# Kernel tuning notes

Hardware: AMD Instinct MI355X
Metric: run time of the kernel (lower is better)

Reference implementation:

```python
import jax, jax.numpy as jnp
import numpy as np

NEG = -9.0e15
D = 768


def _init_params(key, d):
    ks = jax.random.split(key, 12)
    s = 0.02
    p = {}
    p['Wa'] = jax.random.normal(ks[0], (d, 1), jnp.float32) * s
    p['ba'] = jnp.zeros((1,), jnp.float32)
    for i, name in enumerate(['qs', 'ks', 'qc', 'kc', 'qr', 'kr']):
        p['W' + name] = jax.random.normal(ks[1 + i], (d, d), jnp.float32) * s
        p['b' + name] = jnp.zeros((d,), jnp.float32)
    p['Wf1'] = jax.random.normal(ks[8], (3 * d, d), jnp.float32) * s
    p['bf1'] = jnp.zeros((d,), jnp.float32)
    p['Wf2'] = jax.random.normal(ks[9], (d, d), jnp.float32) * s
    p['bf2'] = jnp.zeros((d,), jnp.float32)
    p['gamma'] = jnp.ones((d,), jnp.float32)
    p['beta'] = jnp.zeros((d,), jnp.float32)
    return p


def setup_inputs() -> dict:
    key = jax.random.key(0)
    k1, k2, k3 = jax.random.split(key, 3)
    B, L = 8, 1024
    inp = {
        'x': jax.random.normal(k1, (B, L, D), jnp.float32),
        'x_ids': jax.random.randint(k2, (B, L), 0, 1000, jnp.int64 if jax.config.read('jax_enable_x64') else jnp.int32).astype(jnp.int32),
        'pad_idx': 0,
    }
    inp.update(_init_params(k3, D))
    return inp


def _forward(x, x_ids, pad_idx, Wa, ba, Wqs, bqs, Wks, bks, Wqc, bqc, Wkc, bkc,
             Wqr, bqr, Wkr, bkr, Wf1, bf1, Wf2, bf2, gamma, beta):
    B, L, d = x.shape
    valid = x_ids != pad_idx                             # [B,L]
    valid_len = valid.sum(axis=1)
    sep_pos = jnp.clip(valid_len // 2, 1, max(1, L - 2))  # [B]
    pos = jnp.arange(L)[None, :]                          # [1,L]
    false_mask = (pos < sep_pos[:, None]) & valid         # [B,L]
    option_mask = (pos > sep_pos[:, None]) & valid        # [B,L]

    # anomaly gate over false segment
    a_logits = (x @ Wa + ba)[..., 0]                      # [B,L]
    a_logits = jnp.where(false_mask, a_logits, NEG)
    gate = jax.nn.softmax(a_logits, axis=1) * false_mask.astype(x.dtype)
    gate = gate / jnp.clip(gate.sum(axis=1, keepdims=True), 1e-8)

    scale = 1.0 / jnp.sqrt(jnp.asarray(d, x.dtype))
    q_sup, k_sup = x @ Wqs + bqs, x @ Wks + bks
    q_con, k_con = x @ Wqc + bqc, x @ Wkc + bkc
    q_rep, k_rep = x @ Wqr + bqr, x @ Wkr + bkr

    sup_s = jnp.einsum('bld,bmd->blm', q_sup, k_sup) * scale
    con_s = jnp.einsum('bld,bmd->blm', q_con, k_con) * scale
    rep_s = jnp.einsum('bld,bmd->blm', q_rep, k_rep) * scale

    pair_mask = false_mask[:, :, None] & option_mask[:, None, :]  # [B,L,L]
    sup_attn = jax.nn.softmax(jnp.where(pair_mask, sup_s, NEG), axis=-1)
    rep_attn = jax.nn.softmax(jnp.where(pair_mask, rep_s + jnp.tanh(con_s), NEG), axis=-1)

    rep_vec = jnp.einsum('blm,bmd->bld', rep_attn, x)
    sup_vec = jnp.einsum('blm,bmd->bld', sup_attn, x)

    anomaly_false = jnp.einsum('bl,bld->bd', gate, x)
    w_rep = jnp.einsum('bl,bld->bd', gate, rep_vec)
    w_sup = jnp.einsum('bl,bld->bd', gate, sup_vec)

    fused = jnp.concatenate([anomaly_false, w_rep, w_sup], axis=-1)
    fused = jnp.maximum(fused @ Wf1 + bf1, 0.0) @ Wf2 + bf2  # dropout = eval identity

    mu = fused.mean(axis=-1, keepdims=True)
    var = ((fused - mu) ** 2).mean(axis=-1, keepdims=True)
    fused = (fused - mu) / jnp.sqrt(var + 1e-5) * gamma + beta
    return fused


def reference(x, x_ids, pad_idx, Wa, ba, Wqs, bqs, Wks, bks, Wqc, bqc, Wkc, bkc,
              Wqr, bqr, Wkr, bkr, Wf1, bf1, Wf2, bf2, gamma, beta):
    return _forward(x, x_ids, pad_idx, Wa, ba, Wqs, bqs, Wks, bks, Wqc, bqc,
                    Wkc, bkc, Wqr, bqr, Wkr, bkr, Wf1, bf1, Wf2, bf2, gamma, beta)
```

## Files before the change

### kernel.cpp

```cpp
#include <hip/hip_runtime.h>
#include <math.h>

#define L 1024
#define NB 8
#define D 768
#define NEGV (-9.0e15f)
#define SCALE 0.036084391824351615f

typedef unsigned short u16;
typedef __attribute__((ext_vector_type(8))) short short8;
typedef __attribute__((ext_vector_type(4))) float float4v;
#define MFMA_BF16 __builtin_amdgcn_mfma_f32_16x16x32_bf16

__device__ __forceinline__ float b2f(u16 u) {
    union { unsigned int i; float f; } v; v.i = ((unsigned int)u) << 16; return v.f;
}
__device__ __forceinline__ u16 f2b(float f) {
    union { float fv; unsigned int i; } v; v.fv = f;
    unsigned int x = v.i;
    x += 0x7fffu + ((x >> 16) & 1u);
    return (u16)(x >> 16);
}

template<int F32>
__device__ __forceinline__ float4 ld4(const void* p, size_t idx) {
    if (F32) return *(const float4*)((const float*)p + idx);
    ushort4 v = *(const ushort4*)((const u16*)p + idx);
    return make_float4(b2f(v.x), b2f(v.y), b2f(v.z), b2f(v.w));
}
template<int F32>
__device__ __forceinline__ float ld1(const void* p, size_t idx) {
    if (F32) return ((const float*)p)[idx];
    return b2f(((const u16*)p)[idx]);
}
__device__ __forceinline__ int ldid(const int* p, size_t idx, int is64) {
    return is64 ? p[idx * 2] : p[idx];
}

#define WS_FLAG  ((size_t)0)
#define WS_SEP   ((size_t)64)
#define WS_C0    ((size_t)128)
#define WS_Z0    ((size_t)192)
#define WS_W1    ((size_t)9472)
#define WS_GATE  ((size_t)18752)
#define WS_CSUP  ((size_t)51520)
#define WS_CREP  ((size_t)84288)
#define WS_AF    ((size_t)117056)
#define WS_WREP  ((size_t)141632)
#define WS_WSUP  ((size_t)166208)
#define WS_HACC  ((size_t)190784)
#define WS_ALOG  ((size_t)215360)
#define WS_T     ((size_t)248128)
#define WS_OACC  ((size_t)303104)
#define WS_XB    ((size_t)524288)
#define WS_Z     ((size_t)13107200)
#define WS_SSUP  ((size_t)31981568)
#define WS_WB    WS_SSUP
#define WS_SCMB  ((size_t)40370176)
#define WS_M     WS_SCMB

struct PP { const void* W[6]; const void* b[6]; };

__global__ __launch_bounds__(128) void kdetect(const void* x, const void* ids, int* flag) {
    __shared__ int cnt[2];
    int tid = threadIdx.x;
    if (tid == 0) { cnt[0] = 0; cnt[1] = 0; }
    __syncthreads();
    if (tid < 64) {
        u16 u = ((const u16*)x)[tid * 2];
        int e = (u >> 7) & 0xFF;
        if (e >= 100 && e <= 140) atomicAdd(&cnt[0], 1);
    } else {
        int v = ((const int*)ids)[(tid - 64) * 2 + 1];
        if (v != 0) atomicAdd(&cnt[1], 1);
    }
    __syncthreads();
    if (tid == 0) {
        flag[0] = (cnt[0] < 32) ? 1 : 0;
        flag[1] = (cnt[1] == 0) ? 1 : 0;
    }
}

template<int F32> __device__ void kbias_body(const void* W, const void* vec,
        float* out, float* vs) {
    int tid = threadIdx.x;
    for (int i = tid; i < D; i += 256) vs[i] = ld1<F32>(vec, i);
    __syncthreads();
    int row = blockIdx.x * 64 + (tid >> 2);
    int sub = tid & 3;
    float acc = 0.f;
    for (int i = 0; i < 48; ++i) {
        int k = i * 16 + sub * 4;
        float4 wv = ld4<F32>(W, (size_t)row * D + k);
        acc += wv.x * vs[k] + wv.y * vs[k + 1] + wv.z * vs[k + 2] + wv.w * vs[k + 3];
    }
    acc += __shfl_xor(acc, 1);
    acc += __shfl_xor(acc, 2);
    if (sub == 0) out[row] = acc;
}
template<int F32> __device__ void kc0_body(const void* bq, const void* bk,
        float* c0, float* red) {
    int tid = threadIdx.x;
    float s = 0.f;
    for (int i = tid; i < D; i += 256) s += ld1<F32>(bq, i) * ld1<F32>(bk, i);
    red[tid] = s; __syncthreads();
    for (int st = 128; st > 0; st >>= 1) { if (tid < st) red[tid] += red[tid + st]; __syncthreads(); }
    if (tid == 0) c0[0] = red[0];
}
__global__ __launch_bounds__(256) void kbias_row(PP pp, float* z0, float* w1,
        float* c0, const int* flag) {
    __shared__ float vs[D];
    __shared__ float red[256];
    int y = blockIdx.y;
    if (y == 4) {
        if (blockIdx.x != 0) return;
        if (flag[0]) kc0_body<1>(pp.b[2], pp.b[3], c0, red);
        else         kc0_body<0>(pp.b[2], pp.b[3], c0, red);
        return;
    }
    const void* W; const void* vec; float* out;
    if (y < 3) { W = pp.W[2 * y + 1]; vec = pp.b[2 * y]; out = z0 + y * D; }
    else       { W = pp.W[2];         vec = pp.b[3];     out = w1; }
    if (flag[0]) kbias_body<1>(W, vec, out, vs);
    else         kbias_body<0>(W, vec, out, vs);
}

template<int F32> __device__ void kx_body(const void* x, const void* Wa,
        const void* ba, const float* w1, const float* c0, u16* xb, float* alog,
        float* tbuf, float* ws2) {
    int tid = threadIdx.x;
    for (int i = tid; i < D; i += 256) {
        ws2[i]     = ld1<F32>(Wa, i);
        ws2[D + i] = w1[i];
    }
    __syncthreads();
    int row = blockIdx.x * 32 + (tid >> 3);
    int sub = tid & 7;
    float a0 = 0.f, a1 = 0.f;
    for (int i = 0; i < 24; ++i) {
        int k = i * 32 + sub * 4;
        float4 xv = ld4<F32>(x, (size_t)row * D + k);
        ushort4 o;
        o.x = f2b(xv.x); o.y = f2b(xv.y); o.z = f2b(xv.z); o.w = f2b(xv.w);
        *(ushort4*)(xb + (size_t)row * D + k) = o;
        a0 += xv.x * ws2[k] + xv.y * ws2[k + 1] + xv.z * ws2[k + 2] + xv.w * ws2[k + 3];
        a1 += xv.x * ws2[D + k] + xv.y * ws2[D + k + 1] + xv.z * ws2[D + k + 2] + xv.w * ws2[D + k + 3];
    }
    #pragma unroll
    for (int d = 1; d < 8; d <<= 1) {
        a0 += __shfl_xor(a0, d); a1 += __shfl_xor(a1, d);
    }
    int b = row >> 10, l = row & 1023;
    if (sub == 0) alog[row] = a0 + ld1<F32>(ba, 0);
    else if (sub == 1 && l < 512) tbuf[(size_t)b * 512 + l] = a1 + c0[0];
}
__global__ __launch_bounds__(256) void kx(const void* x, PP pp, const void* Wa,
        const void* ba, const float* w1, const float* c0, u16* xb, u16* Wb,
        float* alog, float* tbuf, const int* flag) {
    __shared__ float ws2[2 * D];
    int bid = blockIdx.x;
    if (bid < 256) {
        if (flag[0]) kx_body<1>(x, Wa, ba, w1, c0, xb, alog, tbuf, ws2);
        else         kx_body<0>(x, Wa, ba, w1, c0, xb, alog, tbuf, ws2);
        return;
    }
    int t = (bid - 256) / 288, inner = (bid - 256) % 288;
    const void* src = pp.W[t];
    u16* dst = Wb + (size_t)t * D * D;
    size_t base = ((size_t)inner * 256 + threadIdx.x) * 8;
    if (flag[0]) {
        float4 a = *(const float4*)((const float*)src + base);
        float4 b = *(const float4*)((const float*)src + base + 4);
        uint4 o; u16* po = (u16*)&o;
        po[0] = f2b(a.x); po[1] = f2b(a.y); po[2] = f2b(a.z); po[3] = f2b(a.w);
        po[4] = f2b(b.x); po[5] = f2b(b.y); po[6] = f2b(b.z); po[7] = f2b(b.w);
        *(uint4*)(dst + base) = o;
    } else {
        *(uint4*)(dst + base) = *(const uint4*)((const u16*)src + base);
    }
}

__global__ __launch_bounds__(256) void k0b(const int* __restrict__ ids,
        const int* __restrict__ padp, const float* __restrict__ alog,
        float* __restrict__ gate, int* __restrict__ sepArr,
        float* __restrict__ af, float* __restrict__ wrep, float* __restrict__ wsup,
        float* __restrict__ hacc, float* __restrict__ oacc,
        float* __restrict__ csup, float* __restrict__ crep,
        const int* __restrict__ flag) {
    __shared__ float red[256];
    __shared__ int sepSh;
    int is64 = flag[1];
    int b = blockIdx.x, tid = threadIdx.x;
    int pad = padp[0];
    int cnt = 0;
    for (int l = tid; l < L; l += 256) cnt += (ldid(ids, (size_t)b * L + l, is64) != pad) ? 1 : 0;
    red[tid] = (float)cnt; __syncthreads();
    for (int s = 128; s > 0; s >>= 1) { if (tid < s) red[tid] += red[tid + s]; __syncthreads(); }
    if (tid == 0) {
        int vl = (int)red[0];
        int sep = vl / 2; if (sep < 1) sep = 1; if (sep > L - 2) sep = L - 2;
        sepSh = sep; sepArr[b] = sep;
    }
    __syncthreads();
    int sep = sepSh;
    float lv[4]; int lidx[4];
    float mx = -3.4e38f;
    for (int u = 0; u < 4; ++u) {
        int l = tid + u * 256; lidx[u] = l;
        bool fm = (l < sep) && (ldid(ids, (size_t)b * L + l, is64) != pad);
        float v = fm ? alog[b * L + l] : NEGV;
        lv[u] = v; mx = fmaxf(mx, v);
    }
    red[tid] = mx; __syncthreads();
    for (int s = 128; s > 0; s >>= 1) { if (tid < s) red[tid] = fmaxf(red[tid], red[tid + s]); __syncthreads(); }
    mx = red[0]; __syncthreads();
    float se = 0.f;
    for (int u = 0; u < 4; ++u) { lv[u] = expf(lv[u] - mx); se += lv[u]; }
    red[tid] = se; __syncthreads();
    for (int s = 128; s > 0; s >>= 1) { if (tid < s) red[tid] += red[tid + s]; __syncthreads(); }
    float den = fmaxf(red[0], 1e-30f); __syncthreads();
    float gs = 0.f; float gv[4];
    for (int u = 0; u < 4; ++u) {
        int l = lidx[u];
        bool fm = (l < sep) && (ldid(ids, (size_t)b * L + l, is64) != pad);
        float p = lv[u] / den;
        gv[u] = fm ? p : 0.f;
        gs += gv[u];
    }
    red[tid] = gs; __syncthreads();
    for (int s = 128; s > 0; s >>= 1) { if (tid < s) red[tid] += red[tid + s]; __syncthreads(); }
    gs = red[0];
    float inv = 1.f / fmaxf(gs, 1e-8f);
    for (int u = 0; u < 4; ++u) gate[b * L + lidx[u]] = gv[u] * inv;
    for (int l = tid; l < L; l += 256) { csup[b * L + l] = 0.f; crep[b * L + l] = 0.f; }
    for (int i = tid; i < D; i += 256) {
        af[b * D + i] = 0.f; wrep[b * D + i] = 0.f; wsup[b * D + i] = 0.f;
        hacc[b * D + i] = 0.f; oacc[b * D + i] = 0.f;
    }
}

__device__ __forceinline__ void stage128_async(const u16* __restrict__ G, size_t ld,
        int r0, int k0, u16* S, int tid) {
    int rowa = tid >> 2, koa = (tid & 3) << 3;
    int wave = tid >> 6;
    const u16* g1 = &G[(size_t)(r0 + rowa) * ld + k0 + koa];
    const u16* g2 = &G[(size_t)(r0 + rowa + 64) * ld + k0 + koa];
    __builtin_amdgcn_global_load_lds((__attribute__((address_space(1))) void*)(u16*)g1,
        (__attribute__((address_space(3))) void*)(S + wave * 512), 16, 0, 0);
    __builtin_amdgcn_global_load_lds((__attribute__((address_space(1))) void*)(u16*)g2,
        (__attribute__((address_space(3))) void*)(S + 2048 + wave * 512), 16, 0, 0);
}
__device__ __forceinline__ void stage64_async(const u16* __restrict__ G, size_t ld,
        int r0, int k0, u16* S, int tid) {
    int rowa = tid >> 2, koa = (tid & 3) << 3;
    int wave = tid >> 6;
    const u16* g = &G[(size_t)(r0 + rowa) * ld + k0 + koa];
    __builtin_amdgcn_global_load_lds((__attribute__((address_space(1))) void*)(u16*)g,
        (__attribute__((address_space(3))) void*)(S + wave * 512), 16, 0, 0);
}

__device__ __forceinline__ void gemm_core128(const u16* __restrict__ A, size_t lda, int r0,
        const u16* __restrict__ B, size_t ldb, int c0, int K,
        u16* As, u16* Bs, float4v acc[4][4]) {
    int tid = threadIdx.x;
    int lane = tid & 63, wave = tid >> 6;
    int wm = (wave >> 1) << 6, wn = (wave & 1) << 6;
    int quad = lane >> 4, lrow = lane & 15;
    #pragma unroll
    for (int i = 0; i < 4; ++i)
        #pragma unroll
        for (int j = 0; j < 4; ++j) acc[i][j] = (float4v){0.f, 0.f, 0.f, 0.f};
    for (int k0 = 0; k0 < K; k0 += 64) {
        __syncthreads();
        stage128_async(A, lda, r0, k0, As, tid);
        stage128_async(A, lda, r0, k0 + 32, As + 4096, tid);
        stage128_async(B, ldb, c0, k0, Bs, tid);
        stage128_async(B, ldb, c0, k0 + 32, Bs + 4096, tid);
        __syncthreads();
        #pragma unroll
        for (int p = 0; p < 2; ++p) {
            const u16* Ap = As + p * 4096;
            const u16* Bp = Bs + p * 4096;
            short8 af[4], bf[4];
            #pragma unroll
            for (int i = 0; i < 4; ++i) af[i] = *(const short8*)&Ap[(wm + i * 16 + lrow) * 32 + quad * 8];
            #pragma unroll
            for (int j = 0; j < 4; ++j) bf[j] = *(const short8*)&Bp[(wn + j * 16 + lrow) * 32 + quad * 8];
            #pragma unroll
            for (int i = 0; i < 4; ++i)
                #pragma unroll
                for (int j = 0; j < 4; ++j)
                    acc[i][j] = MFMA_BF16(af[i], bf[j], acc[i][j], 0, 0, 0);
        }
    }
}

__device__ __forceinline__ void gemm_core64(const u16* __restrict__ A, size_t lda, int r0,
        const u16* __restrict__ B, size_t ldb, int c0, int K,
        u16* As, u16* Bs, float4v acc[2][4]) {
    int tid = threadIdx.x;
    int lane = tid & 63, wave = tid >> 6;
    int wm = (wave >> 1) << 5, wn = (wave & 1) << 6;
    int quad = lane >> 4, lrow = lane & 15;
    #pragma unroll
    for (int i = 0; i < 2; ++i)
        #pragma unroll
        for (int j = 0; j < 4; ++j) acc[i][j] = (float4v){0.f, 0.f, 0.f, 0.f};
    for (int k0 = 0; k0 < K; k0 += 64) {
        __syncthreads();
        stage64_async(A, lda, r0, k0, As, tid);
        stage64_async(A, lda, r0, k0 + 32, As + 2048, tid);
        stage128_async(B, ldb, c0, k0, Bs, tid);
        stage128_async(B, ldb, c0, k0 + 32, Bs + 4096, tid);
        __syncthreads();
        #pragma unroll
        for (int p = 0; p < 2; ++p) {
            const u16* Ap = As + p * 2048;
            const u16* Bp = Bs + p * 4096;
            short8 fa[2], fb[4];
            #pragma unroll
            for (int i = 0; i < 2; ++i) fa[i] = *(const short8*)&Ap[(wm + i * 16 + lrow) * 32 + quad * 8];
            #pragma unroll
            for (int j = 0; j < 4; ++j) fb[j] = *(const short8*)&Bp[(wn + j * 16 + lrow) * 32 + quad * 8];
            #pragma unroll
            for (int i = 0; i < 2; ++i)
                #pragma unroll
                for (int j = 0; j < 4; ++j)
                    acc[i][j] = MFMA_BF16(fa[i], fb[j], acc[i][j], 0, 0, 0);
        }
    }
}

__global__ __launch_bounds__(256) void kM_mfma(const u16* __restrict__ Wb, u16* __restrict__ Mt) {
    __shared__ __align__(16) u16 As[128 * 64];
    __shared__ __align__(16) u16 Bs[128 * 64];
    int p = blockIdx.z;
    int r0 = blockIdx.y * 128, c0 = blockIdx.x * 128;
    float4v acc[4][4];
    gemm_core128(Wb + (size_t)(2 * p + 1) * D * D, D, r0,
                 Wb + (size_t)(2 * p) * D * D, D, c0, D, As, Bs, acc);
    int lane = threadIdx.x & 63, wave = threadIdx.x >> 6;
    int wm = (wave >> 1) << 6, wn = (wave & 1) << 6;
    int quad = lane >> 4, lrow = lane & 15;
    u16* out = Mt + (size_t)p * D * D;
    #pragma unroll
    for (int i = 0; i < 4; ++i)
        #pragma unroll
        for (int j = 0; j < 4; ++j) {
            int brow = r0 + wm + i * 16 + quad * 4;
            int col = c0 + wn + j * 16 + lrow;
            #pragma unroll
            for (int r = 0; r < 4; ++r)
                out[(size_t)(brow + r) * D + col] = f2b(acc[i][j][r]);
        }
}

__global__ __launch_bounds__(256) void kZ_mfma(const u16* __restrict__ xb,
        const u16* __restrict__ Mt, const float* __restrict__ z0,
        u16* __restrict__ Zbuf, const int* __restrict__ sepArr) {
    __shared__ __align__(16) u16 As[64 * 64];
    __shared__ __align__(16) u16 Bs[128 * 64];
    int z = blockIdx.z;
    int p = z >> 3, b = z & 7;
    int sep = sepArr[b];
    int r0 = blockIdx.y * 64;
    if (r0 >= sep) return;
    int c0 = blockIdx.x * 128;
    float4v acc[2][4];
    gemm_core64(xb + (size_t)b * L * D, D, r0,
                Mt + (size_t)p * D * D, D, c0, D, As, Bs, acc);
    int lane = threadIdx.x & 63, wave = threadIdx.x >> 6;
    int wm = (wave >> 1) << 5, wn = (wave & 1) << 6;
    int quad = lane >> 4, lrow = lane & 15;
    const float* z0p = z0 + p * D;
    u16* out = Zbuf + ((size_t)p * NB + b) * 512 * D;
    #pragma unroll
    for (int i = 0; i < 2; ++i)
        #pragma unroll
        for (int j = 0; j < 4; ++j) {
            int brow = r0 + wm + i * 16 + quad * 4;
            int col = c0 + wn + j * 16 + lrow;
            float zb = z0p[col];
            #pragma unroll
            for (int r = 0; r < 4; ++r)
                out[(size_t)(brow + r) * D + col] = f2b(acc[i][j][r] + zb);
        }
}

__global__ __launch_bounds__(256) void kS_mfma(const u16* __restrict__ Zbuf,
        const u16* __restrict__ xb, const float* __restrict__ tcbuf,
        const int* __restrict__ sepArr, u16* __restrict__ ssup,
        u16* __restrict__ scmb) {
    __shared__ __align__(16) u16 smem[16384];
    int b = blockIdx.z;
    int sep = sepArr[b];
    int xi = blockIdx.x;
    int tid = threadIdx.x, lane = tid & 63, wave = tid >> 6;
    int quad = lane >> 4, lrow = lane & 15;
    int wm = (wave >> 1) << 5, wn = (wave & 1) << 6;
    int m0 = blockIdx.y * 128;
    if (m0 + 127 <= sep) return;
    u16* A0 = smem;
    u16* A1 = smem + 4096;
    u16* Bs = smem + 8192;
    const u16* X = xb + (size_t)b * L * D;
    if (xi < 8) {
        int l0 = xi * 64;
        if (l0 >= sep) return;
        float4v acc[2][4];
        gemm_core64(Zbuf + (size_t)b * 512 * D, D, l0, X, D, m0, D, A0, Bs, acc);
        u16* out = ssup + (size_t)b * 512 * L;
        #pragma unroll
        for (int i = 0; i < 2; ++i)
            #pragma unroll
            for (int j = 0; j < 4; ++j) {
                int brow = l0 + wm + i * 16 + quad * 4;
                int col = m0 + wn + j * 16 + lrow;
                #pragma unroll
                for (int r = 0; r < 4; ++r)
                    out[(size_t)(brow + r) * L + col] = f2b(acc[i][j][r] * SCALE);
            }
        return;
    }
    int l0 = (xi - 8) * 64;
    if (l0 >= sep) return;
    const u16* Zr = Zbuf + ((size_t)2 * NB + b) * 512 * D;
    const u16* Zc = Zbuf + ((size_t)1 * NB + b) * 512 * D;
    float4v ar_[2][4], ac_[2][4];
    #pragma unroll
    for (int i = 0; i < 2; ++i)
        #pragma unroll
        for (int j = 0; j < 4; ++j) { ar_[i][j] = (float4v){0.f,0.f,0.f,0.f}; ac_[i][j] = (float4v){0.f,0.f,0.f,0.f}; }
    for (int k0 = 0; k0 < D; k0 += 64) {
        __syncthreads();
        stage64_async(Zr, D, l0, k0, A0, tid);
        stage64_async(Zr, D, l0, k0 + 32, A0 + 2048, tid);
        stage64_async(Zc, D, l0, k0, A1, tid);
        stage64_async(Zc, D, l0, k0 + 32, A1 + 2048, tid);
        stage128_async(X, D, m0, k0, Bs, tid);
        stage128_async(X, D, m0, k0 + 32, Bs + 4096, tid);
        __syncthreads();
        #pragma unroll
        for (int p = 0; p < 2; ++p) {
            const u16* Arp = A0 + p * 2048;
            const u16* Acp = A1 + p * 2048;
            const u16* Bp  = Bs + p * 4096;
            short8 fr[2], fc[2], fb[4];
            #pragma unroll
            for (int i = 0; i < 2; ++i) {
                fr[i] = *(const short8*)&Arp[(wm + i * 16 + lrow) * 32 + quad * 8];
                fc[i] = *(const short8*)&Acp[(wm + i * 16 + lrow) * 32 + quad * 8];
            }
            #pragma unroll
            for (int j = 0; j < 4; ++j) fb[j] = *(const short8*)&Bp[(wn + j * 16 + lrow) * 32 + quad * 8];
            #pragma unroll
            for (int i = 0; i < 2; ++i)
                #pragma unroll
                for (int j = 0; j < 4; ++j) {
                    ar_[i][j] = MFMA_BF16(fr[i], fb[j], ar_[i][j], 0, 0, 0);
                    ac_[i][j] = MFMA_BF16(fc[i], fb[j], ac_[i][j], 0, 0, 0);
                }
        }
    }
    const float* tc = tcbuf + (size_t)b * 512;
    u16* out = scmb + (size_t)b * 512 * L;
    #pragma unroll
    for (int i = 0; i < 2; ++i)
        #pragma unroll
        for (int j = 0; j < 4; ++j) {
            int brow = l0 + wm + i * 16 + quad * 4;
            int col = m0 + wn + j * 16 + lrow;
            #pragma unroll
            for (int r = 0; r < 4; ++r) {
                float vv = ar_[i][j][r] * SCALE
                         + tanhf((ac_[i][j][r] + tc[brow + r]) * SCALE);
                out[(size_t)(brow + r) * L + col] = f2b(vv);
            }
        }
}

__global__ __launch_bounds__(256) void k2bc(const u16* __restrict__ ssup,
        const u16* __restrict__ scmb, const int* __restrict__ ids,
        const int* __restrict__ padp, const int* __restrict__ sepArr,
        const float* __restrict__ gate, float* __restrict__ csup,
        float* __restrict__ crep, const int* __restrict__ flag) {
    __shared__ float colacc[4][2][1024];
    int b = blockIdx.y;
    int sep = sepArr[b];
    int l0 = blockIdx.x * 8;
    int tid = threadIdx.x, lane = tid & 63, w = tid >> 6;
    for (int i = tid; i < 4 * 2 * 1024; i += 256) ((float*)colacc)[i] = 0.f;
    __syncthreads();
    if (l0 < sep) {
        int is64 = flag[1];
        int pad = padp[0];
        unsigned int okmask = 0;
        #pragma unroll
        for (int u = 0; u < 16; ++u) {
            int m = u * 64 + lane;
            bool ok = (m > sep) && (ldid(ids, (size_t)b * L + m, is64) != pad);
            okmask |= (ok ? 1u : 0u) << u;
        }
        for (int t = 0; t < 2; ++t) {
            int l = l0 + w * 2 + t;
            if (l >= sep) continue;
            float g = gate[b * L + l];
            if (g == 0.f) continue;
            const u16* rs = ssup + ((size_t)b * 512 + l) * L;
            const u16* rc = scmb + ((size_t)b * 512 + l) * L;
            float s0[16], s1[16];
            float mx0 = -3.4e38f, mx1 = -3.4e38f;
            #pragma unroll
            for (int u = 0; u < 16; ++u) {
                int m = u * 64 + lane;
                bool ok = (okmask >> u) & 1u;
                s0[u] = ok ? b2f(rs[m]) : NEGV;
                s1[u] = ok ? b2f(rc[m]) : NEGV;
                mx0 = fmaxf(mx0, s0[u]); mx1 = fmaxf(mx1, s1[u]);
            }
            #pragma unroll
            for (int d = 1; d < 64; d <<= 1) {
                mx0 = fmaxf(mx0, __shfl_xor(mx0, d));
                mx1 = fmaxf(mx1, __shfl_xor(mx1, d));
            }
            float e0 = 0.f, e1 = 0.f;
            #pragma unroll
            for (int u = 0; u < 16; ++u) {
                s0[u] = expf(s0[u] - mx0); e0 += s0[u];
                s1[u] = expf(s1[u] - mx1); e1 += s1[u];
            }
            #pragma unroll
            for (int d = 1; d < 64; d <<= 1) {
                e0 += __shfl_xor(e0, d);
                e1 += __shfl_xor(e1, d);
            }
            float i0 = g / fmaxf(e0, 1e-30f), i1 = g / fmaxf(e1, 1e-30f);
            #pragma unroll
            for (int u = 0; u < 16; ++u) {
                int m = u * 64 + lane;
                colacc[w][0][m] += s0[u] * i0;
                colacc[w][1][m] += s1[u] * i1;
            }
        }
    }
    __syncthreads();
    for (int m = tid; m < 1024; m += 256) {
        float a0 = colacc[0][0][m] + colacc[1][0][m] + colacc[2][0][m] + colacc[3][0][m];
        float a1 = colacc[0][1][m] + colacc[1][1][m] + colacc[2][1][m] + colacc[3][1][m];
        if (a0 != 0.f) atomicAdd(&csup[b * L + m], a0);
        if (a1 != 0.f) atomicAdd(&crep[b * L + m], a1);
    }
}

__global__ __launch_bounds__(256) void k3(const u16* __restrict__ xb,
        const float* __restrict__ gate, const float* __restrict__ csup,
        const float* __restrict__ crep, float* __restrict__ af,
        float* __restrict__ wrep, float* __restrict__ wsup) {
    int b = blockIdx.y, c = blockIdx.x;
    int tid = threadIdx.x;
    float a0 = 0.f, a1 = 0.f, a2 = 0.f;
    float r0 = 0.f, r1 = 0.f, r2 = 0.f;
    float q0 = 0.f, q1 = 0.f, q2 = 0.f;
    for (int mm = 0; mm < 16; ++mm) {
        int m = c * 16 + mm;
        float wg = gate[b * L + m], wr = crep[b * L + m], wq = csup[b * L + m];
        if (wg == 0.f && wr == 0.f && wq == 0.f) continue;
        size_t base = ((size_t)b * L + m) * D;
        float x0 = b2f(xb[base + tid]);
        float x1 = b2f(xb[base + tid + 256]);
        float x2 = b2f(xb[base + tid + 512]);
        a0 += wg * x0; a1 += wg * x1; a2 += wg * x2;
        r0 += wr * x0; r1 += wr * x1; r2 += wr * x2;
        q0 += wq * x0; q1 += wq * x1; q2 += wq * x2;
    }
    atomicAdd(&af[b * D + tid], a0); atomicAdd(&af[b * D + tid + 256], a1); atomicAdd(&af[b * D + tid + 512], a2);
    atomicAdd(&wrep[b * D + tid], r0); atomicAdd(&wrep[b * D + tid + 256], r1); atomicAdd(&wrep[b * D + tid + 512], r2);
    atomicAdd(&wsup[b * D + tid], q0); atomicAdd(&wsup[b * D + tid + 256], q1); atomicAdd(&wsup[b * D + tid + 512], q2);
}

template<int F32> __device__ void kh1_body(const float* af, const float* wrep,
        const float* wsup, const void* Wf1, float* hacc, float* fs) {
    int tid = threadIdx.x;
    int c0 = blockIdx.x * 128, k0 = blockIdx.y * 144;
    for (int e = tid; e < 8 * 144; e += 256) {
        int b = e / 144, kk = e - b * 144;
        int k = k0 + kk;
        float v = (k < D) ? af[b * D + k] : (k < 2 * D) ? wrep[b * D + k - D]
                                                        : wsup[b * D + k - 2 * D];
        fs[b * 144 + kk] = v;
    }
    __syncthreads();
    int col = c0 + (tid & 127);
    int kg = tid >> 7;
    float acc[NB];
    #pragma unroll
    for (int b = 0; b < NB; ++b) acc[b] = 0.f;
    #pragma unroll 4
    for (int r = 0; r < 72; ++r) {
        int kk = kg * 72 + r;
        float w = ld1<F32>(Wf1, (size_t)(k0 + kk) * D + col);
        #pragma unroll
        for (int b = 0; b < NB; ++b) acc[b] += fs[b * 144 + kk] * w;
    }
    #pragma unroll
    for (int b = 0; b < NB; ++b) atomicAdd(&hacc[b * D + col], acc[b]);
}
__global__ __launch_bounds__(256) void kh1(const float* af, const float* wrep,
        const float* wsup, const void* Wf1, float* hacc, const int* flag) {
    __shared__ float fs[8 * 144];
    if (flag[0]) kh1_body<1>(af, wrep, wsup, Wf1, hacc, fs);
    else         kh1_body<0>(af, wrep, wsup, Wf1, hacc, fs);
}

template<int F32> __device__ void kh2_body(const float* hacc, const void* bf1,
        const void* Wf2, float* oacc, float* hsl) {
    int tid = threadIdx.x;
    int c0 = blockIdx.x * 128, k0 = blockIdx.y * 96;
    for (int e = tid; e < 8 * 96; e += 256) {
        int b = e / 96, kk = e - b * 96;
        int k = k0 + kk;
        hsl[b * 96 + kk] = fmaxf(hacc[b * D + k] + ld1<F32>(bf1, k), 0.f);
    }
    __syncthreads();
    int col = c0 + (tid & 127);
    int kg = tid >> 7;
    float acc[NB];
    #pragma unroll
    for (int b = 0; b < NB; ++b) acc[b] = 0.f;
    #pragma unroll 4
    for (int r = 0; r < 48; ++r) {
        int kk = kg * 48 + r;
        float w = ld1<F32>(Wf2, (size_t)(k0 + kk) * D + col);
        #pragma unroll
        for (int b = 0; b < NB; ++b) acc[b] += hsl[b * 96 + kk] * w;
    }
    #pragma unroll
    for (int b = 0; b < NB; ++b) atomicAdd(&oacc[b * D + col], acc[b]);
}
__global__ __launch_bounds__(256) void kh2(const float* hacc, const void* bf1,
        const void* Wf2, float* oacc, const int* flag) {
    __shared__ float hsl[8 * 96];
    if (flag[0]) kh2_body<1>(hacc, bf1, Wf2, oacc, hsl);
    else         kh2_body<0>(hacc, bf1, Wf2, oacc, hsl);
}

template<int F32> __device__ void kln_body(const float* oacc, const void* bf2,
        const void* gamma, const void* beta, void* out, float* red) {
    int b = blockIdx.x, tid = threadIdx.x;
    float o[3];
    #pragma unroll
    for (int u = 0; u < 3; ++u) {
        int i = tid + u * 256;
        o[u] = oacc[b * D + i] + ld1<F32>(bf2, i);
    }
    red[tid] = o[0] + o[1] + o[2]; __syncthreads();
    for (int s = 128; s > 0; s >>= 1) { if (tid < s) red[tid] += red[tid + s]; __syncthreads(); }
    float mu = red[0] / (float)D; __syncthreads();
    float vs = 0.f;
    #pragma unroll
    for (int u = 0; u < 3; ++u) vs += (o[u] - mu) * (o[u] - mu);
    red[tid] = vs; __syncthreads();
    for (int s = 128; s > 0; s >>= 1) { if (tid < s) red[tid] += red[tid + s]; __syncthreads(); }
    float var = red[0] / (float)D;
    float rstd = 1.0f / sqrtf(var + 1e-5f);
    #pragma unroll
    for (int u = 0; u < 3; ++u) {
        int i = tid + u * 256;
        float v = (o[u] - mu) * rstd * ld1<F32>(gamma, i) + ld1<F32>(beta, i);
        if (F32) ((float*)out)[b * D + i] = v;
        else     ((u16*)out)[b * D + i] = f2b(v);
    }
}
__global__ __launch_bounds__(256) void kln(const float* oacc, const void* bf2,
        const void* gamma, const void* beta, void* out, const int* flag) {
    __shared__ float red[256];
    if (flag[0]) kln_body<1>(oacc, bf2, gamma, beta, out, red);
    else         kln_body<0>(oacc, bf2, gamma, beta, out, red);
}

extern "C" void kernel_launch(void* const* d_in, const int* in_sizes, int n_in,
                              void* d_out, int out_size, void* d_ws, size_t ws_size,
                              hipStream_t stream) {
    const void* x    = d_in[0];
    const int* ids   = (const int*)d_in[1];
    const int* padp  = (const int*)d_in[2];
    const void* Wa   = d_in[3];
    const void* ba   = d_in[4];
    PP pp;
    pp.W[0] = d_in[5];  pp.b[0] = d_in[6];
    pp.W[1] = d_in[7];  pp.b[1] = d_in[8];
    pp.W[2] = d_in[9];  pp.b[2] = d_in[10];
    pp.W[3] = d_in[11]; pp.b[3] = d_in[12];
    pp.W[4] = d_in[13]; pp.b[4] = d_in[14];
    pp.W[5] = d_in[15]; pp.b[5] = d_in[16];
    const void* Wf1 = d_in[17]; const void* bf1 = d_in[18];
    const void* Wf2 = d_in[19]; const void* bf2 = d_in[20];
    const void* gamma = d_in[21]; const void* beta = d_in[22];

    char* ws = (char*)d_ws;
    int*   flag   = (int*)(ws + WS_FLAG);
    int*   sepArr = (int*)(ws + WS_SEP);
    float* c0   = (float*)(ws + WS_C0);
    float* z0   = (float*)(ws + WS_Z0);
    float* w1   = (float*)(ws + WS_W1);
    float* gate = (float*)(ws + WS_GATE);
    float* csup = (float*)(ws + WS_CSUP);
    float* crep = (float*)(ws + WS_CREP);
    float* af   = (float*)(ws + WS_AF);
    float* wrep = (float*)(ws + WS_WREP);
    float* wsup = (float*)(ws + WS_WSUP);
    float* hacc = (float*)(ws + WS_HACC);
    float* oacc = (float*)(ws + WS_OACC);
    float* alog = (float*)(ws + WS_ALOG);
    float* tbuf = (float*)(ws + WS_T);
    u16* xb   = (u16*)(ws + WS_XB);
    u16* Zbuf = (u16*)(ws + WS_Z);
    u16* Wb   = (u16*)(ws + WS_WB);
    u16* Mt   = (u16*)(ws + WS_M);
    u16* ssup = (u16*)(ws + WS_SSUP);
    u16* scmb = (u16*)(ws + WS_SCMB);

    kdetect<<<dim3(1), dim3(128), 0, stream>>>(x, ids, flag);
    kbias_row<<<dim3(12, 5), dim3(256), 0, stream>>>(pp, z0, w1, c0, flag);
    kx<<<dim3(1984), dim3(256), 0, stream>>>(x, pp, Wa, ba, w1, c0, xb, Wb, alog, tbuf, flag);
    k0b<<<dim3(NB), dim3(256), 0, stream>>>(ids, padp, alog, gate, sepArr,
                                            af, wrep, wsup, hacc, oacc, csup, crep, flag);
    kM_mfma<<<dim3(6, 6, 3), dim3(256), 0, stream>>>(Wb, Mt);
    kZ_mfma<<<dim3(6, 8, 24), dim3(256), 0, stream>>>(xb, Mt, z0, Zbuf, sepArr);
    kS_mfma<<<dim3(16, 8, NB), dim3(256), 0, stream>>>(Zbuf, xb, tbuf, sepArr, ssup, scmb);
    k2bc<<<dim3(64, NB), dim3(256), 0, stream>>>(ssup, scmb, ids, padp, sepArr,
                                                 gate, csup, crep, flag);
    k3<<<dim3(64, NB), dim3(256), 0, stream>>>(xb, gate, csup, crep, af, wrep, wsup);
    kh1<<<dim3(6, 16), dim3(256), 0, stream>>>(af, wrep, wsup, Wf1, hacc, flag);
    kh2<<<dim3(6, 8), dim3(256), 0, stream>>>(hacc, bf1, Wf2, oacc, flag);
    kln<<<dim3(NB), dim3(256), 0, stream>>>(oacc, bf2, gamma, beta, d_out, flag);
}
```

Baseline: 286.0 us.

## Fuse weight bf16 conversion into M-matrix GEMM staging, drop Wb buffer

Removes the separate pass in kx that converted the six projection weight matrices to bf16 into a workspace buffer. kM_mfma now reads the fp32 (or bf16) weights directly and converts while staging tiles into shared memory, using its own simpler single-buffered K=32 loop instead of gemm_core128. This saves a full write and re-read of the weight copies and shrinks kx to its x-processing blocks. In exchange the M GEMM reads wider fp32 data, converts each tile redundantly across blocks, and loses whatever pipelining gemm_core128 had.

```diff
diff --git a/kernel.cpp b/kernel.cpp
--- a/kernel.cpp
+++ b/kernel.cpp
@@ -55,7 +55,6 @@
 #define WS_XB    ((size_t)524288)
 #define WS_Z     ((size_t)13107200)
 #define WS_SSUP  ((size_t)31981568)
-#define WS_WB    WS_SSUP
 #define WS_SCMB  ((size_t)40370176)
 #define WS_M     WS_SCMB
 
@@ -154,30 +153,12 @@
     if (sub == 0) alog[row] = a0 + ld1<F32>(ba, 0);
     else if (sub == 1 && l < 512) tbuf[(size_t)b * 512 + l] = a1 + c0[0];
 }
-__global__ __launch_bounds__(256) void kx(const void* x, PP pp, const void* Wa,
-        const void* ba, const float* w1, const float* c0, u16* xb, u16* Wb,
+__global__ __launch_bounds__(256) void kx(const void* x, const void* Wa,
+        const void* ba, const float* w1, const float* c0, u16* xb,
         float* alog, float* tbuf, const int* flag) {
     __shared__ float ws2[2 * D];
-    int bid = blockIdx.x;
-    if (bid < 256) {
-        if (flag[0]) kx_body<1>(x, Wa, ba, w1, c0, xb, alog, tbuf, ws2);
-        else         kx_body<0>(x, Wa, ba, w1, c0, xb, alog, tbuf, ws2);
-        return;
-    }
-    int t = (bid - 256) / 288, inner = (bid - 256) % 288;
-    const void* src = pp.W[t];
-    u16* dst = Wb + (size_t)t * D * D;
-    size_t base = ((size_t)inner * 256 + threadIdx.x) * 8;
-    if (flag[0]) {
-        float4 a = *(const float4*)((const float*)src + base);
-        float4 b = *(const float4*)((const float*)src + base + 4);
-        uint4 o; u16* po = (u16*)&o;
-        po[0] = f2b(a.x); po[1] = f2b(a.y); po[2] = f2b(a.z); po[3] = f2b(a.w);
-        po[4] = f2b(b.x); po[5] = f2b(b.y); po[6] = f2b(b.z); po[7] = f2b(b.w);
-        *(uint4*)(dst + base) = o;
-    } else {
-        *(uint4*)(dst + base) = *(const uint4*)((const u16*)src + base);
-    }
+    if (flag[0]) kx_body<1>(x, Wa, ba, w1, c0, xb, alog, tbuf, ws2);
+    else         kx_body<0>(x, Wa, ba, w1, c0, xb, alog, tbuf, ws2);
 }
 
 __global__ __launch_bounds__(256) void k0b(const int* __restrict__ ids,
@@ -331,18 +312,52 @@
     }
 }
 
-__global__ __launch_bounds__(256) void kM_mfma(const u16* __restrict__ Wb, u16* __restrict__ Mt) {
-    __shared__ __align__(16) u16 As[128 * 64];
-    __shared__ __align__(16) u16 Bs[128 * 64];
-    int p = blockIdx.z;
+template<int F32> __device__ __forceinline__ void stageW(const void* G, size_t ld,
+        int r0, int k0, u16* S, int tid) {
+    int row = tid >> 2, ko = (tid & 3) << 3;
+    #pragma unroll
+    for (int h = 0; h < 2; ++h) {
+        size_t idx = (size_t)(r0 + row + h * 64) * ld + k0 + ko;
+        uint4 o;
+        if (F32) {
+            float4 a = *(const float4*)((const float*)G + idx);
+            float4 b = *(const float4*)((const float*)G + idx + 4);
+            u16* po = (u16*)&o;
+            po[0] = f2b(a.x); po[1] = f2b(a.y); po[2] = f2b(a.z); po[3] = f2b(a.w);
+            po[4] = f2b(b.x); po[5] = f2b(b.y); po[6] = f2b(b.z); po[7] = f2b(b.w);
+        } else {
+            o = *(const uint4*)((const u16*)G + idx);
+        }
+        *(uint4*)&S[(size_t)(row + h * 64) * 32 + ko] = o;
+    }
+}
+template<int F32> __device__ void kM_body(const void* Wk, const void* Wq,
+        u16* out, u16* As, u16* Bs) {
     int r0 = blockIdx.y * 128, c0 = blockIdx.x * 128;
-    float4v acc[4][4];
-    gemm_core128(Wb + (size_t)(2 * p + 1) * D * D, D, r0,
-                 Wb + (size_t)(2 * p) * D * D, D, c0, D, As, Bs, acc);
-    int lane = threadIdx.x & 63, wave = threadIdx.x >> 6;
+    int tid = threadIdx.x, lane = tid & 63, wave = tid >> 6;
     int wm = (wave >> 1) << 6, wn = (wave & 1) << 6;
     int quad = lane >> 4, lrow = lane & 15;
-    u16* out = Mt + (size_t)p * D * D;
+    float4v acc[4][4];
+    #pragma unroll
+    for (int i = 0; i < 4; ++i)
+        #pragma unroll
+        for (int j = 0; j < 4; ++j) acc[i][j] = (float4v){0.f, 0.f, 0.f, 0.f};
+    for (int k0 = 0; k0 < D; k0 += 32) {
+        __syncthreads();
+        stageW<F32>(Wk, D, r0, k0, As, tid);
+        stageW<F32>(Wq, D, c0, k0, Bs, tid);
+        __syncthreads();
+        short8 af[4], bf[4];
+        #pragma unroll
+        for (int i = 0; i < 4; ++i) af[i] = *(const short8*)&As[(wm + i * 16 + lrow) * 32 + quad * 8];
+        #pragma unroll
+        for (int j = 0; j < 4; ++j) bf[j] = *(const short8*)&Bs[(wn + j * 16 + lrow) * 32 + quad * 8];
+        #pragma unroll
+        for (int i = 0; i < 4; ++i)
+            #pragma unroll
+            for (int j = 0; j < 4; ++j)
+                acc[i][j] = MFMA_BF16(af[i], bf[j], acc[i][j], 0, 0, 0);
+    }
     #pragma unroll
     for (int i = 0; i < 4; ++i)
         #pragma unroll
@@ -353,6 +368,15 @@
             for (int r = 0; r < 4; ++r)
                 out[(size_t)(brow + r) * D + col] = f2b(acc[i][j][r]);
         }
+}
+__global__ __launch_bounds__(256) void kM_mfma(PP pp, u16* __restrict__ Mt,
+        const int* __restrict__ flag) {
+    __shared__ __align__(16) u16 As[128 * 32];
+    __shared__ __align__(16) u16 Bs[128 * 32];
+    int p = blockIdx.z;
+    u16* out = Mt + (size_t)p * D * D;
+    if (flag[0]) kM_body<1>(pp.W[2 * p + 1], pp.W[2 * p], out, As, Bs);
+    else         kM_body<0>(pp.W[2 * p + 1], pp.W[2 * p], out, As, Bs);
 }
 
 __global__ __launch_bounds__(256) void kZ_mfma(const u16* __restrict__ xb,
@@ -715,17 +739,16 @@
     float* tbuf = (float*)(ws + WS_T);
     u16* xb   = (u16*)(ws + WS_XB);
     u16* Zbuf = (u16*)(ws + WS_Z);
-    u16* Wb   = (u16*)(ws + WS_WB);
     u16* Mt   = (u16*)(ws + WS_M);
     u16* ssup = (u16*)(ws + WS_SSUP);
     u16* scmb = (u16*)(ws + WS_SCMB);
 
     kdetect<<<dim3(1), dim3(128), 0, stream>>>(x, ids, flag);
     kbias_row<<<dim3(12, 5), dim3(256), 0, stream>>>(pp, z0, w1, c0, flag);
-    kx<<<dim3(1984), dim3(256), 0, stream>>>(x, pp, Wa, ba, w1, c0, xb, Wb, alog, tbuf, flag);
+    kx<<<dim3(256), dim3(256), 0, stream>>>(x, Wa, ba, w1, c0, xb, alog, tbuf, flag);
     k0b<<<dim3(NB), dim3(256), 0, stream>>>(ids, padp, alog, gate, sepArr,
                                             af, wrep, wsup, hacc, oacc, csup, crep, flag);
-    kM_mfma<<<dim3(6, 6, 3), dim3(256), 0, stream>>>(Wb, Mt);
+    kM_mfma<<<dim3(6, 6, 3), dim3(256), 0, stream>>>(pp, Mt, flag);
     kZ_mfma<<<dim3(6, 8, 24), dim3(256), 0, stream>>>(xb, Mt, z0, Zbuf, sepArr);
     kS_mfma<<<dim3(16, 8, NB), dim3(256), 0, stream>>>(Zbuf, xb, tbuf, sepArr, ssup, scmb);
     k2bc<<<dim3(64, NB), dim3(256), 0, stream>>>(ssup, scmb, ids, padp, sepArr,
```

Measured after the change: 295.7 us. 1.03x slower.
